# Kernel tuning notes

Measured on AMD Instinct MI355X. Metric: run time of the kernel, lower is better.

## Reference

```python
import jax, jax.numpy as jnp
import numpy as np

D = 128
NQ, NP = 2048, 256
H1, H2 = 128, 64


def setup_inputs() -> dict:
    key = jax.random.key(0)
    ks = jax.random.split(key, 8)
    s1 = 1.0 / np.sqrt(2 * D)
    s2 = 1.0 / np.sqrt(H1)
    s3 = 1.0 / np.sqrt(H2)
    return {
        "query_features": jax.random.normal(ks[0], (NQ, D), dtype=jnp.float32),
        "prototypes": jax.random.normal(ks[1], (NP, D), dtype=jnp.float32),
        # torch Linear layout: W [out, in], y = x @ W.T + b
        "W1": jax.random.uniform(ks[2], (H1, 2 * D), jnp.float32, -s1, s1),
        "b1": jax.random.uniform(ks[3], (H1,), jnp.float32, -s1, s1),
        "W2": jax.random.uniform(ks[4], (H2, H1), jnp.float32, -s2, s2),
        "b2": jax.random.uniform(ks[5], (H2,), jnp.float32, -s2, s2),
        "W3": jax.random.uniform(ks[6], (1, H2), jnp.float32, -s3, s3),
        "b3": jax.random.uniform(ks[7], (1,), jnp.float32, -s3, s3),
    }


def reference(query_features, prototypes, W1, b1, W2, b2, W3, b3):
    d = query_features.shape[1]
    # concat([q, p]) @ W1.T == q @ W1[:, :d].T + p @ W1[:, d:].T  (avoids
    # materializing the [Nq, Np, 2d] pair tensor the torch loop builds)
    qh = query_features @ W1[:, :d].T          # [Nq, H1]
    ph = prototypes @ W1[:, d:].T              # [Np, H1]
    h1 = jax.nn.relu(qh[:, None, :] + ph[None, :, :] + b1)      # [Nq, Np, H1]
    h2 = jax.nn.relu(jnp.einsum("qph,oh->qpo", h1, W2) + b2)    # [Nq, Np, H2]
    evidence = jax.nn.softplus(jnp.einsum("qpo,o->qp", h2, W3[0]) + b3[0])  # [Nq, Np]
    alpha = evidence + 1.0
    uncertainty = 1.0 / alpha
    # squared euclidean distance (cdist(p=2) ** 2)
    qn = jnp.sum(query_features ** 2, axis=1, keepdims=True)    # [Nq, 1]
    pn = jnp.sum(prototypes ** 2, axis=1)[None, :]              # [1, Np]
    base = jnp.maximum(qn + pn - 2.0 * (query_features @ prototypes.T), 0.0)
    confidence_weights = 1.0 / (uncertainty + 1e-8)
    return base * confidence_weights
```

## Files before the change

kernel.cpp:

```cpp
#include <hip/hip_runtime.h>
#include <hip/hip_bf16.h>
#include <hip/hip_fp16.h>

#define D1   128
#define NQ   2048
#define NP   256
#define H1   128
#define H2   64

typedef __attribute__((ext_vector_type(8))) _Float16 f16x8;
typedef __attribute__((ext_vector_type(2))) __fp16   h16x2;
typedef __attribute__((ext_vector_type(4))) float    f32x4;

#define L_PF   0
#define L_W1Q  65536
#define L_W1P  98304
#define L_W2   131072
#define L_QF   147456
#define L_QH   149504
#define LDS_TOTAL 151552

static __device__ __forceinline__ f16x8 cvt8(float4 a, float4 b) {
    f16x8 f;
    f[0] = (_Float16)a.x; f[1] = (_Float16)a.y;
    f[2] = (_Float16)a.z; f[3] = (_Float16)a.w;
    f[4] = (_Float16)b.x; f[5] = (_Float16)b.y;
    f[6] = (_Float16)b.z; f[7] = (_Float16)b.w;
    return f;
}
static __device__ __forceinline__ float sqsum8(f16x8 v, float acc) {
    union { f16x8 f; h16x2 h[4]; } u; u.f = v;
    acc = __builtin_amdgcn_fdot2(u.h[0], u.h[0], acc, false);
    acc = __builtin_amdgcn_fdot2(u.h[1], u.h[1], acc, false);
    acc = __builtin_amdgcn_fdot2(u.h[2], u.h[2], acc, false);
    acc = __builtin_amdgcn_fdot2(u.h[3], u.h[3], acc, false);
    return acc;
}
#define FRAG(base, row, ks) \
    (*(const f16x8*)((base) + ((((row) * 256 + (ks) * 64 + g * 16)) ^ (((row) & 7) << 4))))

__global__ void __launch_bounds__(512, 2)
fused_kernel(const float* __restrict__ q, const float* __restrict__ p,
             const float* __restrict__ W1, const float* __restrict__ b1,
             const float* __restrict__ W2, const float* __restrict__ b2,
             const float* __restrict__ w3, const float* __restrict__ b3,
             float* __restrict__ out) {
    extern __shared__ char lds[];
    char* pf_s  = lds + L_PF;
    char* w1q_s = lds + L_W1Q;
    char* w1p_s = lds + L_W1P;
    char* w2_s  = lds + L_W2;
    char* qf_s  = lds + L_QF;
    char* qh_s  = lds + L_QH;

    int tid = threadIdx.x, lane = tid & 63, w = tid >> 6;
    int lo = lane & 15, g = lane >> 4;
    int wp = w & 3, qh2 = w >> 2;
    int q0 = blockIdx.x * 8;

    #pragma unroll
    for (int it = 0; it < 8; ++it) {
        int j8 = (it * 512 + tid) * 8;
        int row = j8 >> 7;
        const float* src = p + j8;
        *(f16x8*)(pf_s + ((j8 * 2) ^ ((row & 7) << 4))) =
            cvt8(*(const float4*)src, *(const float4*)(src + 4));
    }
    #pragma unroll
    for (int it = 0; it < 8; ++it) {
        int j8 = (it * 512 + tid) * 8;
        int row = j8 >> 8, col = j8 & 255;
        const float* src = W1 + j8;
        f16x8 v = cvt8(*(const float4*)src, *(const float4*)(src + 4));
        char* base = (col < 128) ? w1q_s : w1p_s;
        *(f16x8*)(base + ((row * 256 + (col & 127) * 2) ^ ((row & 7) << 4))) = v;
    }
    #pragma unroll
    for (int it = 0; it < 2; ++it) {
        int j8 = (it * 512 + tid) * 8;
        int row = j8 >> 7;
        const float* src = W2 + j8;
        *(f16x8*)(w2_s + ((j8 * 2) ^ ((row & 7) << 4))) =
            cvt8(*(const float4*)src, *(const float4*)(src + 4));
    }
    if (tid < 128) {
        int j8 = tid * 8;
        int row = j8 >> 7;
        const float* src = q + q0 * D1 + j8;
        *(f16x8*)(qf_s + ((j8 * 2) ^ ((row & 7) << 4))) =
            cvt8(*(const float4*)src, *(const float4*)(src + 4));
    }
    __syncthreads();

    f16x8 Praw[4][4];
    float psq[4];
    #pragma unroll
    for (int n = 0; n < 4; ++n) {
        int prow = wp * 64 + n * 16 + lo;
        psq[n] = 0.f;
        #pragma unroll
        for (int ks = 0; ks < 4; ++ks) {
            Praw[n][ks] = FRAG(pf_s, prow, ks);
            psq[n] = sqsum8(Praw[n][ks], psq[n]);
        }
        psq[n] += __shfl_xor(psq[n], 16);
        psq[n] += __shfl_xor(psq[n], 32);
    }
    f16x8 Adist[4];
    float asq = 0.f;
    {
        int qrow = qh2 * 4 + (lo & 3);
        #pragma unroll
        for (int ks = 0; ks < 4; ++ks) {
            Adist[ks] = FRAG(qf_s, qrow, ks);
            asq = sqsum8(Adist[ks], asq);
        }
        asq += __shfl_xor(asq, 16);
        asq += __shfl_xor(asq, 32);
    }
    f16x8 Aq[4], Bq[4];
    {
        int hrow = w * 16 + lo, qrow2 = lo & 7;
        #pragma unroll
        for (int ks = 0; ks < 4; ++ks) {
            Aq[ks] = FRAG(w1q_s, hrow, ks);
            Bq[ks] = FRAG(qf_s, qrow2, ks);
        }
    }
    const f32x4 Zv = (f32x4){0.f, 0.f, 0.f, 0.f};
    const f16x8 zz = {};
    const h16x2 z2 = {};
    float4 b1v = *(const float4*)(b1 + w * 16 + g * 4);
    __syncthreads();

    {
        f32x4 Cq = Zv;
        #pragma unroll
        for (int ks = 0; ks < 4; ++ks)
            Cq = __builtin_amdgcn_mfma_f32_16x16x32_f16(Aq[ks], Bq[ks], Cq, 0, 0, 0);
        if (lo < 8) {
            union { h16x2 h[2]; uint2 v; } pk;
            pk.h[0] = __builtin_amdgcn_cvt_pkrtz(Cq[0] + b1v.x, Cq[1] + b1v.y);
            pk.h[1] = __builtin_amdgcn_cvt_pkrtz(Cq[2] + b1v.z, Cq[3] + b1v.w);
            *(uint2*)(qh_s + lo * 256 + w * 32 + g * 8) = pk.v;
        }
    }
    float bse[4];
    {
        f32x4 Cd[4];
        #pragma unroll
        for (int n = 0; n < 4; ++n) {
            Cd[n] = Zv;
            #pragma unroll
            for (int ks = 0; ks < 4; ++ks)
                Cd[n] = __builtin_amdgcn_mfma_f32_16x16x32_f16(Adist[ks], Praw[n][ks], Cd[n], 0, 0, 0);
        }
        float pnm = (g == 0) ? psq[0] : (g == 1) ? psq[1] : (g == 2) ? psq[2] : psq[3];
        #pragma unroll
        for (int qq = 0; qq < 4; ++qq) {
            float qn = __shfl(asq, qq);
            float dg = (g == 0) ? Cd[0][qq] : (g == 1) ? Cd[1][qq]
                     : (g == 2) ? Cd[2][qq] : Cd[3][qq];
            bse[qq] = fmaxf(qn + pnm - 2.f * dg, 0.f);
        }
    }
    #pragma unroll
    for (int hp = 0; hp < 2; ++hp) {
        f16x8 Ap[2][4];
        #pragma unroll
        for (int ht = 0; ht < 2; ++ht) {
            int h = (qh2 * 4 + hp * 2 + ht) * 16 + lo;
            #pragma unroll
            for (int ks = 0; ks < 4; ++ks)
                Ap[ht][ks] = FRAG(w1p_s, h, ks);
        }
        #pragma unroll
        for (int n = 0; n < 4; ++n) {
            f32x4 Cp0 = Zv, Cp1 = Zv;
            #pragma unroll
            for (int ks = 0; ks < 4; ++ks) {
                Cp0 = __builtin_amdgcn_mfma_f32_16x16x32_f16(Ap[0][ks], Praw[n][ks], Cp0, 0, 0, 0);
                Cp1 = __builtin_amdgcn_mfma_f32_16x16x32_f16(Ap[1][ks], Praw[n][ks], Cp1, 0, 0, 0);
            }
            int pp = wp * 64 + n * 16 + lo;
            #pragma unroll
            for (int ht = 0; ht < 2; ++ht) {
                f32x4 Cp = ht ? Cp1 : Cp0;
                int h0 = (qh2 * 4 + hp * 2 + ht) * 16 + g * 4;
                union { h16x2 h[2]; uint2 v; } pk;
                pk.h[0] = __builtin_amdgcn_cvt_pkrtz(Cp[0], Cp[1]);
                pk.h[1] = __builtin_amdgcn_cvt_pkrtz(Cp[2], Cp[3]);
                *(uint2*)(pf_s + ((pp * 256 + h0 * 2) ^ ((pp & 7) << 4))) = pk.v;
            }
        }
    }
    __syncthreads();

    f16x8 P[4][4];
    #pragma unroll
    for (int n = 0; n < 4; ++n)
        #pragma unroll
        for (int ks = 0; ks < 4; ++ks) {
            int pp = wp * 64 + n * 16 + lo;
            P[n][ks] = FRAG(pf_s, pp, ks);
            asm volatile("" : "+v"(P[n][ks]));
        }
    f16x8 Af[4][4];
    #pragma unroll
    for (int m = 0; m < 4; ++m)
        #pragma unroll
        for (int ks = 0; ks < 4; ++ks) {
            Af[m][ks] = FRAG(w2_s, m * 16 + lo, ks);
            asm volatile("" : "+v"(Af[m][ks]));
        }

    h16x2 b2p[4][2], w3p[4][2];
    #pragma unroll
    for (int m = 0; m < 4; ++m) {
        float4 bb = *(const float4*)(b2 + m * 16 + g * 4);
        float4 ww = *(const float4*)(w3 + m * 16 + g * 4);
        b2p[m][0] = __builtin_amdgcn_cvt_pkrtz(bb.x, bb.y);
        b2p[m][1] = __builtin_amdgcn_cvt_pkrtz(bb.z, bb.w);
        w3p[m][0] = __builtin_amdgcn_cvt_pkrtz(ww.x, ww.y);
        w3p[m][1] = __builtin_amdgcn_cvt_pkrtz(ww.z, ww.w);
    }
    float b3v = b3[0];
    int pmine = wp * 64 + lane;
    int qb = qh2 * 4;

    f16x8 qkr[2][4];
    #pragma unroll
    for (int ks = 0; ks < 4; ++ks)
        qkr[0][ks] = *(const f16x8*)(qh_s + qb * 256 + ks * 64 + g * 16);

    #pragma unroll
    for (int qq = 0; qq < 4; ++qq) {
        float zp[4];
        #pragma unroll
        for (int hh = 0; hh < 2; ++hh) {
            f32x4 C[4][2];
            #pragma unroll
            for (int ks = 0; ks < 4; ++ks) {
                f16x8 B0 = __builtin_elementwise_max(P[2 * hh + 0][ks] + qkr[qq & 1][ks], zz);
                f16x8 B1 = __builtin_elementwise_max(P[2 * hh + 1][ks] + qkr[qq & 1][ks], zz);
                #pragma unroll
                for (int m = 0; m < 4; ++m) {
                    if (ks == 0) {
                        C[m][0] = __builtin_amdgcn_mfma_f32_16x16x32_f16(Af[m][0], B0, Zv, 0, 0, 0);
                        C[m][1] = __builtin_amdgcn_mfma_f32_16x16x32_f16(Af[m][0], B1, Zv, 0, 0, 0);
                    } else {
                        C[m][0] = __builtin_amdgcn_mfma_f32_16x16x32_f16(Af[m][ks], B0, C[m][0], 0, 0, 0);
                        C[m][1] = __builtin_amdgcn_mfma_f32_16x16x32_f16(Af[m][ks], B1, C[m][1], 0, 0, 0);
                    }
                }
            }
            if (hh == 0 && qq + 1 < 4) {
                #pragma unroll
                for (int ks = 0; ks < 4; ++ks)
                    qkr[(qq + 1) & 1][ks] =
                        *(const f16x8*)(qh_s + (qb + qq + 1) * 256 + ks * 64 + g * 16);
            }
            #pragma unroll
            for (int n2 = 0; n2 < 2; ++n2) {
                float sA = 0.f, sB = 0.f;
                #pragma unroll
                for (int m = 0; m < 4; ++m) {
                    h16x2 c01 = __builtin_amdgcn_cvt_pkrtz(C[m][n2][0], C[m][n2][1]);
                    h16x2 c23 = __builtin_amdgcn_cvt_pkrtz(C[m][n2][2], C[m][n2][3]);
                    h16x2 h01 = __builtin_elementwise_max(c01 + b2p[m][0], z2);
                    h16x2 h23 = __builtin_elementwise_max(c23 + b2p[m][1], z2);
                    sA = __builtin_amdgcn_fdot2(h01, w3p[m][0], sA, false);
                    sB = __builtin_amdgcn_fdot2(h23, w3p[m][1], sB, false);
                }
                zp[2 * hh + n2] = sA + sB;
            }
        }
        float sh[4];
        #pragma unroll
        for (int i = 0; i < 4; ++i) sh[i] = __shfl_xor(zp[i], 16);
        #pragma unroll
        for (int i = 0; i < 4; ++i) zp[i] += sh[i];
        #pragma unroll
        for (int i = 0; i < 4; ++i) sh[i] = __shfl_xor(zp[i], 32);
        #pragma unroll
        for (int i = 0; i < 4; ++i) zp[i] += sh[i];

        float z = (g == 0) ? zp[0] : (g == 1) ? zp[1] : (g == 2) ? zp[2] : zp[3];
        z += b3v;
        float sp = fmaxf(z, 0.f) + __logf(1.f + __expf(-fabsf(z)));
        out[(q0 + qb + qq) * NP + pmine] = bse[qq] * (1.f + sp);
    }
}

extern "C" void kernel_launch(void* const* d_in, const int* in_sizes, int n_in,
                              void* d_out, int out_size, void* d_ws, size_t ws_size,
                              hipStream_t stream) {
    const float* q  = (const float*)d_in[0];
    const float* pr = (const float*)d_in[1];
    const float* W1 = (const float*)d_in[2];
    const float* b1 = (const float*)d_in[3];
    const float* W2 = (const float*)d_in[4];
    const float* b2 = (const float*)d_in[5];
    const float* W3 = (const float*)d_in[6];
    const float* b3 = (const float*)d_in[7];
    float* out = (float*)d_out;

    fused_kernel<<<NQ / 8, 512, LDS_TOTAL, stream>>>(q, pr, W1, b1, W2, b2,
                                                     W3, b3, out);
}
```

Before: 22.40 us.

## Pre-cast inputs to swizzled fp16 in workspace and DMA directly into LDS

```diff
diff --git a/kernel.cpp b/kernel.cpp
--- a/kernel.cpp
+++ b/kernel.cpp
@@ -19,6 +19,7 @@
 #define L_QF   147456
 #define L_QH   149504
 #define LDS_TOTAL 151552
+#define WS_Q16 147456
 
 static __device__ __forceinline__ f16x8 cvt8(float4 a, float4 b) {
     f16x8 f;
@@ -36,13 +37,48 @@
     acc = __builtin_amdgcn_fdot2(u.h[3], u.h[3], acc, false);
     return acc;
 }
+static __device__ __forceinline__ void dma16(const void* g, void* l) {
+    __builtin_amdgcn_global_load_lds(
+        (const __attribute__((address_space(1))) void*)g,
+        (__attribute__((address_space(3))) void*)l, 16, 0, 0);
+}
 #define FRAG(base, row, ks) \
     (*(const f16x8*)((base) + ((((row) * 256 + (ks) * 64 + g * 16)) ^ (((row) & 7) << 4))))
 
+__global__ void __launch_bounds__(512)
+prep_cast_kernel(const float* __restrict__ q, const float* __restrict__ p,
+                 const float* __restrict__ W1, const float* __restrict__ W2,
+                 char* __restrict__ wsb) {
+    int o = blockIdx.x * 512 + threadIdx.x;
+    const float* src; char* dst;
+    if (o < 4096) {
+        int row = o >> 4;
+        src = p + o * 8;
+        dst = wsb + ((o * 16) ^ ((row & 7) << 4));
+    } else if (o < 6144) {
+        int oo = o - 4096, row = oo >> 4, c8 = (oo & 15) * 8;
+        src = W1 + row * 256 + c8;
+        dst = wsb + 65536 + ((oo * 16) ^ ((row & 7) << 4));
+    } else if (o < 8192) {
+        int oo = o - 6144, row = oo >> 4, c8 = (oo & 15) * 8;
+        src = W1 + row * 256 + 128 + c8;
+        dst = wsb + 98304 + ((oo * 16) ^ ((row & 7) << 4));
+    } else if (o < 9216) {
+        int oo = o - 8192, row = oo >> 4;
+        src = W2 + oo * 8;
+        dst = wsb + 131072 + ((oo * 16) ^ ((row & 7) << 4));
+    } else {
+        int oo = o - 9216, row = oo >> 4;
+        src = q + oo * 8;
+        dst = wsb + WS_Q16 + ((oo * 16) ^ ((row & 7) << 4));
+    }
+    float4 a = *(const float4*)src, b = *(const float4*)(src + 4);
+    *(f16x8*)dst = cvt8(a, b);
+}
+
 __global__ void __launch_bounds__(512, 2)
-fused_kernel(const float* __restrict__ q, const float* __restrict__ p,
-             const float* __restrict__ W1, const float* __restrict__ b1,
-             const float* __restrict__ W2, const float* __restrict__ b2,
+fused_kernel(const char* __restrict__ wsb,
+             const float* __restrict__ b1, const float* __restrict__ b2,
              const float* __restrict__ w3, const float* __restrict__ b3,
              float* __restrict__ out) {
     extern __shared__ char lds[];
@@ -58,37 +94,15 @@
     int wp = w & 3, qh2 = w >> 2;
     int q0 = blockIdx.x * 8;
 
-    #pragma unroll
-    for (int it = 0; it < 8; ++it) {
-        int j8 = (it * 512 + tid) * 8;
-        int row = j8 >> 7;
-        const float* src = p + j8;
-        *(f16x8*)(pf_s + ((j8 * 2) ^ ((row & 7) << 4))) =
-            cvt8(*(const float4*)src, *(const float4*)(src + 4));
-    }
-    #pragma unroll
-    for (int it = 0; it < 8; ++it) {
-        int j8 = (it * 512 + tid) * 8;
-        int row = j8 >> 8, col = j8 & 255;
-        const float* src = W1 + j8;
-        f16x8 v = cvt8(*(const float4*)src, *(const float4*)(src + 4));
-        char* base = (col < 128) ? w1q_s : w1p_s;
-        *(f16x8*)(base + ((row * 256 + (col & 127) * 2) ^ ((row & 7) << 4))) = v;
-    }
-    #pragma unroll
-    for (int it = 0; it < 2; ++it) {
-        int j8 = (it * 512 + tid) * 8;
-        int row = j8 >> 7;
-        const float* src = W2 + j8;
-        *(f16x8*)(w2_s + ((j8 * 2) ^ ((row & 7) << 4))) =
-            cvt8(*(const float4*)src, *(const float4*)(src + 4));
-    }
-    if (tid < 128) {
-        int j8 = tid * 8;
-        int row = j8 >> 7;
-        const float* src = q + q0 * D1 + j8;
-        *(f16x8*)(qf_s + ((j8 * 2) ^ ((row & 7) << 4))) =
-            cvt8(*(const float4*)src, *(const float4*)(src + 4));
+    const char* qsrc = wsb + WS_Q16 + q0 * 256;
+    #pragma unroll
+    for (int i = 0; i < 19; ++i) {
+        int idx = i * 8 + w;
+        if (idx < 146) {
+            const char* gsc = (idx < 144) ? (wsb + idx * 1024)
+                                          : (qsrc + (idx - 144) * 1024);
+            dma16(gsc + lane * 16, lds + idx * 1024 + lane * 16);
+        }
     }
     __syncthreads();
 
@@ -304,7 +318,8 @@
     const float* W3 = (const float*)d_in[6];
     const float* b3 = (const float*)d_in[7];
     float* out = (float*)d_out;
-
-    fused_kernel<<<NQ / 8, 512, LDS_TOTAL, stream>>>(q, pr, W1, b1, W2, b2,
-                                                     W3, b3, out);
-}
+    char* wsb  = (char*)d_ws;
+
+    prep_cast_kernel<<<82, 512, 0, stream>>>(q, pr, W1, W2, wsb);
+    fused_kernel<<<NQ / 8, 512, LDS_TOTAL, stream>>>(wsb, b1, b2, W3, b3, out);
+}
```

After: 26.14 us. +16.7%, slower.
